# Kernel tuning notes

Measured on AMD Instinct MI355X. Metric: run time of the kernel, lower is better.

Reference implementation:

```python
import jax, jax.numpy as jnp
import numpy as np

B = 8192          # batch_size (pairs of embeddings)
D = 1024          # embedding dim
C = 1024          # number of classes (torch.unique(labels) -> 0..C-1, all present)
EPS = 1e-12       # F.normalize eps


def _normalize(x):
    # F.normalize(x, dim=1): x / max(||x||_2, eps)
    n = jnp.linalg.norm(x, axis=1, keepdims=True)
    return x / jnp.maximum(n, EPS)


def setup_inputs() -> dict:
    key = jax.random.key(0)
    k1, k2, k3 = jax.random.split(key, 3)
    emb_i = jax.random.normal(k1, (B, D), dtype=jnp.float32)
    emb_j = jax.random.normal(k2, (B, D), dtype=jnp.float32)
    # shuffled arange % C guarantees every class id in [0, C) appears,
    # matching torch.unique(labels) == arange(C)
    labels = jax.random.permutation(k3, jnp.arange(B, dtype=jnp.int32) % C).astype(jnp.int64)
    return {"emb_i": emb_i, "emb_j": emb_j, "labels": labels}


def reference(emb_i, emb_j, labels):
    z_i = _normalize(emb_i)  # [B, D]
    z_j = _normalize(emb_j)  # [B, D]

    # vectorized replacement of the per-label python loop:
    # class_prototypes[c] = mean of z_i rows with label c  (segment mean)
    seg_sum = jax.ops.segment_sum(z_i, labels, num_segments=C)                    # [C, D]
    seg_cnt = jax.ops.segment_sum(jnp.ones((B,), z_i.dtype), labels, num_segments=C)  # [C]
    prototypes = seg_sum / seg_cnt[:, None]                                       # [C, D]

    # similarity = 2 - cdist(z_j, prototypes, p=2)
    d2 = (jnp.sum(z_j * z_j, axis=1)[:, None]
          + jnp.sum(prototypes * prototypes, axis=1)[None, :]
          - 2.0 * z_j @ prototypes.T)                                             # [B, C]
    sim = 2.0 - jnp.sqrt(jnp.maximum(d2, 0.0))

    # match_matrix: labels_proto (arange(C)) == labels[:, None]
    match = (jnp.arange(C)[None, :] == labels[:, None]).astype(sim.dtype)         # [B, C]

    # BCEWithLogitsLoss (mean reduction), numerically stable via log_sigmoid
    loss = jnp.mean(-(match * jax.nn.log_sigmoid(sim)
                      + (1.0 - match) * jax.nn.log_sigmoid(-sim)))
    return loss
```

## Files before the change

### kernel.cpp

```cpp
#include <hip/hip_runtime.h>

#define B_N 8192
#define D_N 1024
#define C_N 1024
#define BM 256
#define BN 128
#define BK 64

typedef __attribute__((ext_vector_type(8))) __bf16 bf16x8;
typedef __attribute__((ext_vector_type(16))) float floatx16;

__device__ inline unsigned short f2bf(float f) {
  union { float f; unsigned int u; } cv; cv.f = f;
  unsigned int b = cv.u;
  unsigned int r = (b + 0x7FFFu + ((b >> 16) & 1u)) >> 16;
  return (unsigned short)r;
}
__device__ inline float d4(const float4 a) {
  return a.x * a.x + a.y * a.y + a.z * a.z + a.w * a.w;
}
__device__ inline ushort4 pk4(const float4 v, const float s) {
  ushort4 u;
  u.x = f2bf(v.x * s); u.y = f2bf(v.y * s);
  u.z = f2bf(v.z * s); u.w = f2bf(v.w * s);
  return u;
}

__global__ __launch_bounds__(256) void prep_a(
    const float* __restrict__ emb_j, const int* __restrict__ labels,
    unsigned short* __restrict__ z_j, int* __restrict__ idx,
    float* __restrict__ out) {
  const int t = threadIdx.x;
  const int lane = t & 63;
  const int wid = t >> 6;
  const int b = blockIdx.x;

  if (b == 0 && t == 0) out[0] = 0.0f;

  if (b < 2048) {
    const int row = b * 4 + wid;
    const float4* src = (const float4*)(emb_j + (size_t)row * D_N);
    const float4 v0 = src[lane], v1 = src[lane + 64];
    const float4 v2 = src[lane + 128], v3 = src[lane + 192];
    float ss = d4(v0) + d4(v1) + d4(v2) + d4(v3);
    for (int o = 32; o; o >>= 1) ss += __shfl_xor(ss, o, 64);
    const float inv = 1.0f / fmaxf(sqrtf(ss), 1e-12f);
    ushort4* dst = (ushort4*)(z_j + (size_t)row * D_N);
    dst[lane] = pk4(v0, inv);
    dst[lane + 64] = pk4(v1, inv);
    dst[lane + 128] = pk4(v2, inv);
    dst[lane + 192] = pk4(v3, inv);
  } else {
    __shared__ int cnt[128];
    const int ib = b - 2048;
    for (int i = t; i < 128; i += 256) cnt[i] = 0;
    __syncthreads();
    const int4* lab4 = (const int4*)labels;
    for (int i = 0; i < 8; ++i) {
      const int qv = i * 256 + t;
      const int4 L = lab4[qv];
      const int base = qv * 4;
      if ((L.x >> 7) == ib) idx[L.x * 8 + atomicAdd(&cnt[L.x & 127], 1)] = base;
      if ((L.y >> 7) == ib) idx[L.y * 8 + atomicAdd(&cnt[L.y & 127], 1)] = base + 1;
      if ((L.z >> 7) == ib) idx[L.z * 8 + atomicAdd(&cnt[L.z & 127], 1)] = base + 2;
      if ((L.w >> 7) == ib) idx[L.w * 8 + atomicAdd(&cnt[L.w & 127], 1)] = base + 3;
    }
  }
}

__global__ __launch_bounds__(256) void prep_b(
    const float* __restrict__ emb_i, const int* __restrict__ idx,
    unsigned short* __restrict__ proto, float* __restrict__ p2) {
  __shared__ float sx[4][8];
  const int t = threadIdx.x;
  const int lane = t & 63;
  const int wid = t >> 6;
  const int c = blockIdx.x;

  int li[8];
#pragma unroll
  for (int k = 0; k < 8; ++k) li[k] = idx[c * 8 + k];

  const float* base = emb_i + wid * 256;
  float4 v[8];
  float ss[8];
#pragma unroll
  for (int k = 0; k < 8; ++k) {
    v[k] = ((const float4*)(base + (size_t)li[k] * D_N))[lane];
    ss[k] = d4(v[k]);
  }
#pragma unroll
  for (int k = 0; k < 8; ++k)
    for (int o = 32; o; o >>= 1) ss[k] += __shfl_xor(ss[k], o, 64);
  if (lane == 0) {
#pragma unroll
    for (int k = 0; k < 8; ++k) sx[wid][k] = ss[k];
  }
  __syncthreads();

  float4 a = make_float4(0.f, 0.f, 0.f, 0.f);
#pragma unroll
  for (int k = 0; k < 8; ++k) {
    const float tot = sx[0][k] + sx[1][k] + sx[2][k] + sx[3][k];
    const float iv = 1.0f / fmaxf(sqrtf(tot), 1e-12f);
    a.x += v[k].x * iv; a.y += v[k].y * iv;
    a.z += v[k].z * iv; a.w += v[k].w * iv;
  }
  a.x *= 0.125f; a.y *= 0.125f; a.z *= 0.125f; a.w *= 0.125f;

  float pp = d4(a);
  for (int o = 32; o; o >>= 1) pp += __shfl_xor(pp, o, 64);
  __syncthreads();
  if (lane == 0) sx[wid][0] = pp;
  __syncthreads();
  if (t == 0) p2[c] = sx[0][0] + sx[1][0] + sx[2][0] + sx[3][0];

  ((ushort4*)(proto + (size_t)c * D_N + wid * 256))[lane] = pk4(a, 1.0f);
}

#define GLOAD(gp, lp)                                                        \
  __builtin_amdgcn_global_load_lds(                                          \
      (const __attribute__((address_space(1))) void*)(gp),                   \
      (__attribute__((address_space(3))) void*)(lp), 16, 0, 0)

__global__ __launch_bounds__(512) void gemm_loss_kernel(
    const unsigned short* __restrict__ Zj,
    const unsigned short* __restrict__ P,
    const float* __restrict__ p2,
    const int* __restrict__ labels,
    float* __restrict__ out) {
  __shared__ __align__(16) unsigned short lds[3 * 24576];
  __shared__ float sred[8];

  const int t = threadIdx.x;
  const int lane = t & 63;
  const int wid = t >> 6;
  const int wm = (wid >> 1) * 64;
  const int wn = (wid & 1) * 64;
  const int bm = blockIdx.x;
  const int bn = blockIdx.y;

  floatx16 acc[2][2];
#pragma unroll
  for (int i = 0; i < 2; ++i)
#pragma unroll
    for (int j = 0; j < 2; ++j)
      for (int r = 0; r < 16; ++r) acc[i][j][r] = 0.f;

  const int srow = t >> 3;
  const int g = (t & 7) ^ (srow & 7);
  const unsigned short* Ag = Zj + (size_t)(bm * BM + srow) * D_N + g * 8;
  const unsigned short* Bg = P + (size_t)(bn * BN + srow) * D_N + g * 8;
  unsigned short* const Al0 = (unsigned short*)lds + t * 8;
  unsigned short* const Bl0 = (unsigned short*)lds + 16384 + t * 8;

  const int ar0 = (wm + (lane & 31)) * BK;
  const int ar1 = ar0 + 32 * BK;
  const int br0 = 16384 + (wn + (lane & 31)) * BK;
  const int br1 = br0 + 32 * BK;
  const int h = lane >> 5;
  const int q = lane & 7;

#define STAGE_A(bi, k2)                                                      \
  do {                                                                       \
    unsigned short* _al = Al0 + (bi) * 24576;                                \
    GLOAD(Ag + (size_t)0 * 64 * D_N + (k2), _al + 0 * 4096);                 \
    GLOAD(Ag + (size_t)1 * 64 * D_N + (k2), _al + 1 * 4096);                 \
    GLOAD(Ag + (size_t)2 * 64 * D_N + (k2), _al + 2 * 4096);                 \
  } while (0)
#define STAGE_B(bi, k2)                                                      \
  do {                                                                       \
    unsigned short* _al = Al0 + (bi) * 24576;                                \
    unsigned short* _bl = Bl0 + (bi) * 24576;                                \
    GLOAD(Ag + (size_t)3 * 64 * D_N + (k2), _al + 3 * 4096);                 \
    GLOAD(Bg + (size_t)0 * 64 * D_N + (k2), _bl + 0 * 4096);                 \
    GLOAD(Bg + (size_t)1 * 64 * D_N + (k2), _bl + 1 * 4096);                 \
  } while (0)
#define NOGL ((void)0)

#define PHASE(bi, kkb, GL)                                                   \
  {                                                                          \
    const unsigned short* Lb = (const unsigned short*)lds + (bi) * 24576;    \
    const int s0 = ((((kkb) + 0) * 2 + h) ^ q) << 3;                         \
    const int s1 = ((((kkb) + 1) * 2 + h) ^ q) << 3;                         \
    bf16x8 a0k0 = *(const bf16x8*)(Lb + ar0 + s0);                           \
    bf16x8 a1k0 = *(const bf16x8*)(Lb + ar1 + s0);                           \
    bf16x8 b0k0 = *(const bf16x8*)(Lb + br0 + s0);                           \
    bf16x8 b1k0 = *(const bf16x8*)(Lb + br1 + s0);                           \
    bf16x8 a0k1 = *(const bf16x8*)(Lb + ar0 + s1);                           \
    bf16x8 a1k1 = *(const bf16x8*)(Lb + ar1 + s1);                           \
    bf16x8 b0k1 = *(const bf16x8*)(Lb + br0 + s1);                           \
    bf16x8 b1k1 = *(const bf16x8*)(Lb + br1 + s1);                           \
    GL;                                                                      \
    asm volatile("s_waitcnt lgkmcnt(0)" ::: "memory");                       \
    __builtin_amdgcn_sched_barrier(0);                                       \
    __builtin_amdgcn_s_setprio(1);                                           \
    acc[0][0] = __builtin_amdgcn_mfma_f32_32x32x16_bf16(a0k0, b0k0, acc[0][0], 0, 0, 0); \
    acc[0][1] = __builtin_amdgcn_mfma_f32_32x32x16_bf16(a0k0, b1k0, acc[0][1], 0, 0, 0); \
    acc[1][0] = __builtin_amdgcn_mfma_f32_32x32x16_bf16(a1k0, b0k0, acc[1][0], 0, 0, 0); \
    acc[1][1] = __builtin_amdgcn_mfma_f32_32x32x16_bf16(a1k0, b1k0, acc[1][1], 0, 0, 0); \
    acc[0][0] = __builtin_amdgcn_mfma_f32_32x32x16_bf16(a0k1, b0k1, acc[0][0], 0, 0, 0); \
    acc[0][1] = __builtin_amdgcn_mfma_f32_32x32x16_bf16(a0k1, b1k1, acc[0][1], 0, 0, 0); \
    acc[1][0] = __builtin_amdgcn_mfma_f32_32x32x16_bf16(a1k1, b0k1, acc[1][0], 0, 0, 0); \
    acc[1][1] = __builtin_amdgcn_mfma_f32_32x32x16_bf16(a1k1, b1k1, acc[1][1], 0, 0, 0); \
    __builtin_amdgcn_s_setprio(0);                                           \
    __builtin_amdgcn_sched_barrier(0);                                       \
    __builtin_amdgcn_s_barrier();                                            \
  }

  STAGE_A(0, 0); STAGE_B(0, 0);
  STAGE_A(1, BK); STAGE_B(1, BK);

  int cur = 0;
  for (int kt = 0; kt < 14; ++kt) {
    const int nb = (cur == 0) ? 2 : cur - 1;
    const int k2 = (kt + 2) * BK;
    asm volatile("s_waitcnt vmcnt(6)" ::: "memory");
    __builtin_amdgcn_s_barrier();
    PHASE(cur, 0, STAGE_A(nb, k2));
    PHASE(cur, 2, STAGE_B(nb, k2));
    cur = (cur == 2) ? 0 : cur + 1;
  }
  asm volatile("s_waitcnt vmcnt(6)" ::: "memory");
  __builtin_amdgcn_s_barrier();
  PHASE(cur, 0, NOGL);
  PHASE(cur, 2, NOGL);
  cur = (cur == 2) ? 0 : cur + 1;
  asm volatile("s_waitcnt vmcnt(0)" ::: "memory");
  __builtin_amdgcn_s_barrier();
  PHASE(cur, 0, NOGL);
  PHASE(cur, 2, NOGL);

  const int colbase = bn * BN + wn + (lane & 31);
  float lsum = 0.f;
#pragma unroll
  for (int mb = 0; mb < 2; ++mb) {
    const int rowbase = bm * BM + wm + mb * 32 + 4 * h;
    int labv[16];
#pragma unroll
    for (int reg = 0; reg < 16; ++reg)
      labv[reg] = labels[rowbase + (reg & 3) + 8 * (reg >> 2)];
#pragma unroll
    for (int nb2 = 0; nb2 < 2; ++nb2) {
      const int col = colbase + nb2 * 32;
      const float p2c = p2[col];
#pragma unroll
      for (int reg = 0; reg < 16; ++reg) {
        const float dot = acc[mb][nb2][reg];
        const float d2 = 1.0f + p2c - 2.0f * dot;
        const float s = 2.0f - sqrtf(fmaxf(d2, 0.0f));
        const float e = __expf(-fabsf(s));
        lsum += fmaxf(s, 0.0f) + __logf(1.0f + e) - ((labv[reg] == col) ? s : 0.0f);
      }
    }
  }
  for (int o = 32; o; o >>= 1) lsum += __shfl_xor(lsum, o, 64);
  if (lane == 0) sred[wid] = lsum;
  __syncthreads();
  if (t == 0) {
    float bs = 0.f;
#pragma unroll
    for (int w = 0; w < 8; ++w) bs += sred[w];
    atomicAdd(out, bs * (1.0f / ((float)B_N * (float)C_N)));
  }
}

extern "C" void kernel_launch(void* const* d_in, const int* in_sizes, int n_in,
                              void* d_out, int out_size, void* d_ws, size_t ws_size,
                              hipStream_t stream) {
  const float* emb_i = (const float*)d_in[0];
  const float* emb_j = (const float*)d_in[1];
  const int* labels = (const int*)d_in[2];
  float* out = (float*)d_out;

  char* ws = (char*)d_ws;
  unsigned short* z_j = (unsigned short*)ws;
  unsigned short* proto = (unsigned short*)(ws + (size_t)16777216);
  float* p2 = (float*)(ws + (size_t)18874368);
  int* idx = (int*)(ws + (size_t)18878464);

  prep_a<<<dim3(2056), 256, 0, stream>>>(emb_j, labels, z_j, idx, out);
  prep_b<<<dim3(C_N), 256, 0, stream>>>(emb_i, idx, proto, p2);
  gemm_loss_kernel<<<dim3(B_N / BM, C_N / BN), 512, 0, stream>>>(z_j, proto,
                                                                 p2, labels, out);
}
```

Measured before the change: 131.2 us.

## Shrink GEMM tile to 128x128 with 256 threads and simple double buffering

Halves the M tile from 256 to 128 rows and uses 4 waves per block instead of 8. The triple-buffered, interleaved load/compute pipeline with priority hints becomes a plain two-stage double buffer that issues the next tile's loads before computing the current one. Grid size doubles to 512 blocks and LDS per block drops, which should raise occupancy and fill more CUs. The cost is less reuse of each loaded tile, a simpler schedule with an extra barrier per k-step, and the loss of the fine-grained setprio/sched_barrier control.

```diff
diff --git a/kernel.cpp b/kernel.cpp
--- a/kernel.cpp
+++ b/kernel.cpp
@@ -3,7 +3,7 @@
 #define B_N 8192
 #define D_N 1024
 #define C_N 1024
-#define BM 256
+#define BM 128
 #define BN 128
 #define BK 64
 
@@ -123,14 +123,14 @@
       (const __attribute__((address_space(1))) void*)(gp),                   \
       (__attribute__((address_space(3))) void*)(lp), 16, 0, 0)
 
-__global__ __launch_bounds__(512) void gemm_loss_kernel(
+__global__ __launch_bounds__(256) void gemm_loss_kernel(
     const unsigned short* __restrict__ Zj,
     const unsigned short* __restrict__ P,
     const float* __restrict__ p2,
     const int* __restrict__ labels,
     float* __restrict__ out) {
-  __shared__ __align__(16) unsigned short lds[3 * 24576];
-  __shared__ float sred[8];
+  __shared__ __align__(16) unsigned short lds[2 * 16384];
+  __shared__ float sred[4];
 
   const int t = threadIdx.x;
   const int lane = t & 63;
@@ -152,84 +152,59 @@
   const unsigned short* Ag = Zj + (size_t)(bm * BM + srow) * D_N + g * 8;
   const unsigned short* Bg = P + (size_t)(bn * BN + srow) * D_N + g * 8;
   unsigned short* const Al0 = (unsigned short*)lds + t * 8;
-  unsigned short* const Bl0 = (unsigned short*)lds + 16384 + t * 8;
+  unsigned short* const Bl0 = (unsigned short*)lds + 8192 + t * 8;
 
   const int ar0 = (wm + (lane & 31)) * BK;
   const int ar1 = ar0 + 32 * BK;
-  const int br0 = 16384 + (wn + (lane & 31)) * BK;
+  const int br0 = 8192 + (wn + (lane & 31)) * BK;
   const int br1 = br0 + 32 * BK;
   const int h = lane >> 5;
   const int q = lane & 7;
 
-#define STAGE_A(bi, k2)                                                      \
+#define STAGE(bi, kt)                                                        \
   do {                                                                       \
-    unsigned short* _al = Al0 + (bi) * 24576;                                \
-    GLOAD(Ag + (size_t)0 * 64 * D_N + (k2), _al + 0 * 4096);                 \
-    GLOAD(Ag + (size_t)1 * 64 * D_N + (k2), _al + 1 * 4096);                 \
-    GLOAD(Ag + (size_t)2 * 64 * D_N + (k2), _al + 2 * 4096);                 \
+    const int _bo = (bi) * 16384;                                            \
+    const int _k0 = (kt) * BK;                                               \
+    GLOAD(Ag + (size_t)0 * 32 * D_N + _k0, Al0 + _bo + 0 * 2048);            \
+    GLOAD(Ag + (size_t)1 * 32 * D_N + _k0, Al0 + _bo + 1 * 2048);            \
+    GLOAD(Ag + (size_t)2 * 32 * D_N + _k0, Al0 + _bo + 2 * 2048);            \
+    GLOAD(Ag + (size_t)3 * 32 * D_N + _k0, Al0 + _bo + 3 * 2048);            \
+    GLOAD(Bg + (size_t)0 * 32 * D_N + _k0, Bl0 + _bo + 0 * 2048);            \
+    GLOAD(Bg + (size_t)1 * 32 * D_N + _k0, Bl0 + _bo + 1 * 2048);            \
+    GLOAD(Bg + (size_t)2 * 32 * D_N + _k0, Bl0 + _bo + 2 * 2048);            \
+    GLOAD(Bg + (size_t)3 * 32 * D_N + _k0, Bl0 + _bo + 3 * 2048);            \
   } while (0)
-#define STAGE_B(bi, k2)                                                      \
-  do {                                                                       \
-    unsigned short* _al = Al0 + (bi) * 24576;                                \
-    unsigned short* _bl = Bl0 + (bi) * 24576;                                \
-    GLOAD(Ag + (size_t)3 * 64 * D_N + (k2), _al + 3 * 4096);                 \
-    GLOAD(Bg + (size_t)0 * 64 * D_N + (k2), _bl + 0 * 4096);                 \
-    GLOAD(Bg + (size_t)1 * 64 * D_N + (k2), _bl + 1 * 4096);                 \
-  } while (0)
-#define NOGL ((void)0)
-
-#define PHASE(bi, kkb, GL)                                                   \
+
+#define COMPUTE(bi)                                                          \
   {                                                                          \
-    const unsigned short* Lb = (const unsigned short*)lds + (bi) * 24576;    \
-    const int s0 = ((((kkb) + 0) * 2 + h) ^ q) << 3;                         \
-    const int s1 = ((((kkb) + 1) * 2 + h) ^ q) << 3;                         \
-    bf16x8 a0k0 = *(const bf16x8*)(Lb + ar0 + s0);                           \
-    bf16x8 a1k0 = *(const bf16x8*)(Lb + ar1 + s0);                           \
-    bf16x8 b0k0 = *(const bf16x8*)(Lb + br0 + s0);                           \
-    bf16x8 b1k0 = *(const bf16x8*)(Lb + br1 + s0);                           \
-    bf16x8 a0k1 = *(const bf16x8*)(Lb + ar0 + s1);                           \
-    bf16x8 a1k1 = *(const bf16x8*)(Lb + ar1 + s1);                           \
-    bf16x8 b0k1 = *(const bf16x8*)(Lb + br0 + s1);                           \
-    bf16x8 b1k1 = *(const bf16x8*)(Lb + br1 + s1);                           \
-    GL;                                                                      \
-    asm volatile("s_waitcnt lgkmcnt(0)" ::: "memory");                       \
-    __builtin_amdgcn_sched_barrier(0);                                       \
-    __builtin_amdgcn_s_setprio(1);                                           \
-    acc[0][0] = __builtin_amdgcn_mfma_f32_32x32x16_bf16(a0k0, b0k0, acc[0][0], 0, 0, 0); \
-    acc[0][1] = __builtin_amdgcn_mfma_f32_32x32x16_bf16(a0k0, b1k0, acc[0][1], 0, 0, 0); \
-    acc[1][0] = __builtin_amdgcn_mfma_f32_32x32x16_bf16(a1k0, b0k0, acc[1][0], 0, 0, 0); \
-    acc[1][1] = __builtin_amdgcn_mfma_f32_32x32x16_bf16(a1k0, b1k0, acc[1][1], 0, 0, 0); \
-    acc[0][0] = __builtin_amdgcn_mfma_f32_32x32x16_bf16(a0k1, b0k1, acc[0][0], 0, 0, 0); \
-    acc[0][1] = __builtin_amdgcn_mfma_f32_32x32x16_bf16(a0k1, b1k1, acc[0][1], 0, 0, 0); \
-    acc[1][0] = __builtin_amdgcn_mfma_f32_32x32x16_bf16(a1k1, b0k1, acc[1][0], 0, 0, 0); \
-    acc[1][1] = __builtin_amdgcn_mfma_f32_32x32x16_bf16(a1k1, b1k1, acc[1][1], 0, 0, 0); \
-    __builtin_amdgcn_s_setprio(0);                                           \
-    __builtin_amdgcn_sched_barrier(0);                                       \
-    __builtin_amdgcn_s_barrier();                                            \
-  }
-
-  STAGE_A(0, 0); STAGE_B(0, 0);
-  STAGE_A(1, BK); STAGE_B(1, BK);
+    const unsigned short* Lb = (const unsigned short*)lds + (bi) * 16384;    \
+    _Pragma("unroll") for (int kk = 0; kk < 4; ++kk) {                       \
+      const int swz = ((kk * 2 + h) ^ q) << 3;                               \
+      bf16x8 a0 = *(const bf16x8*)(Lb + ar0 + swz);                          \
+      bf16x8 a1 = *(const bf16x8*)(Lb + ar1 + swz);                          \
+      bf16x8 b0 = *(const bf16x8*)(Lb + br0 + swz);                          \
+      bf16x8 b1 = *(const bf16x8*)(Lb + br1 + swz);                          \
+      acc[0][0] = __builtin_amdgcn_mfma_f32_32x32x16_bf16(a0, b0, acc[0][0], 0, 0, 0); \
+      acc[0][1] = __builtin_amdgcn_mfma_f32_32x32x16_bf16(a0, b1, acc[0][1], 0, 0, 0); \
+      acc[1][0] = __builtin_amdgcn_mfma_f32_32x32x16_bf16(a1, b0, acc[1][0], 0, 0, 0); \
+      acc[1][1] = __builtin_amdgcn_mfma_f32_32x32x16_bf16(a1, b1, acc[1][1], 0, 0, 0); \
+    }                                                                        \
+  }
+
+  STAGE(0, 0);
 
   int cur = 0;
-  for (int kt = 0; kt < 14; ++kt) {
-    const int nb = (cur == 0) ? 2 : cur - 1;
-    const int k2 = (kt + 2) * BK;
-    asm volatile("s_waitcnt vmcnt(6)" ::: "memory");
+  for (int kt = 0; kt < 15; ++kt) {
+    STAGE(cur ^ 1, kt + 1);
+    asm volatile("s_waitcnt vmcnt(8)" ::: "memory");
     __builtin_amdgcn_s_barrier();
-    PHASE(cur, 0, STAGE_A(nb, k2));
-    PHASE(cur, 2, STAGE_B(nb, k2));
-    cur = (cur == 2) ? 0 : cur + 1;
-  }
-  asm volatile("s_waitcnt vmcnt(6)" ::: "memory");
-  __builtin_amdgcn_s_barrier();
-  PHASE(cur, 0, NOGL);
-  PHASE(cur, 2, NOGL);
-  cur = (cur == 2) ? 0 : cur + 1;
+    COMPUTE(cur);
+    __builtin_amdgcn_s_barrier();
+    cur ^= 1;
+  }
   asm volatile("s_waitcnt vmcnt(0)" ::: "memory");
   __builtin_amdgcn_s_barrier();
-  PHASE(cur, 0, NOGL);
-  PHASE(cur, 2, NOGL);
+  COMPUTE(cur);
 
   const int colbase = bn * BN + wn + (lane & 31);
   float lsum = 0.f;
@@ -257,12 +232,9 @@
   for (int o = 32; o; o >>= 1) lsum += __shfl_xor(lsum, o, 64);
   if (lane == 0) sred[wid] = lsum;
   __syncthreads();
-  if (t == 0) {
-    float bs = 0.f;
-#pragma unroll
-    for (int w = 0; w < 8; ++w) bs += sred[w];
-    atomicAdd(out, bs * (1.0f / ((float)B_N * (float)C_N)));
-  }
+  if (t == 0)
+    atomicAdd(out, (sred[0] + sred[1] + sred[2] + sred[3]) *
+                       (1.0f / ((float)B_N * (float)C_N)));
 }
 
 extern "C" void kernel_launch(void* const* d_in, const int* in_sizes, int n_in,
@@ -281,6 +253,6 @@
 
   prep_a<<<dim3(2056), 256, 0, stream>>>(emb_j, labels, z_j, idx, out);
   prep_b<<<dim3(C_N), 256, 0, stream>>>(emb_i, idx, proto, p2);
-  gemm_loss_kernel<<<dim3(B_N / BM, C_N / BN), 512, 0, stream>>>(z_j, proto,
+  gemm_loss_kernel<<<dim3(B_N / BM, C_N / BN), 256, 0, stream>>>(z_j, proto,
                                                                  p2, labels, out);
 }
```

Measured after the change: 132.2 us. No clear change (+0.7%).
